# Kernel tuning notes

Hardware: AMD Instinct MI355X
Metric: run time of the kernel (lower is better)

## Reference

```python
import jax, jax.numpy as jnp
import numpy as np

EPS = 1e-5
K = 20
MAXV = 64


def knn_idx(x, k):
    # x: [B,N,D] -> idx: [B,N,k] (excluding self, matching torch topk of -dist)
    xx = jnp.sum(x * x, axis=-1, keepdims=True)                      # [B,N,1]
    dist = xx - 2.0 * jnp.einsum('bnd,bmd->bnm', x, x) + jnp.swapaxes(xx, 1, 2)
    _, idx = jax.lax.top_k(-dist, k + 1)
    return idx[:, :, 1:]


def edge_conv(x, W, gamma, beta, mean, var, k):
    # x: [B,N,C]; W: [O,2C]; BN in eval mode; max over k neighbors
    idx = knn_idx(x, k)                                              # [B,N,k]
    nbr = jax.vmap(lambda xi, ii: xi[ii])(x, idx)                    # [B,N,k,C]
    ctr = jnp.broadcast_to(x[:, :, None, :], nbr.shape)
    ef = jnp.concatenate([ctr, nbr - ctr], axis=-1)                  # [B,N,k,2C]
    y = jnp.einsum('bnkc,oc->bnko', ef, W)                           # 1x1 conv
    y = (y - mean) * (gamma * jax.lax.rsqrt(var + EPS)) + beta       # BN eval
    y = jnp.where(y >= 0, y, 0.2 * y)                                # LeakyReLU
    return jnp.max(y, axis=2)                                        # [B,N,O]


def setup_inputs() -> dict:
    key = jax.random.key(0)
    ks = jax.random.split(key, 32)
    f32 = jnp.float32
    def w(k_, o, i):
        return jax.random.normal(k_, (o, i), f32) / np.float32(np.sqrt(i))
    def vec(k_, c):
        return jax.random.normal(k_, (c,), f32) * 0.1
    d = {}
    d['x'] = jax.random.normal(ks[0], (4, 8192, 5), f32)
    # EdgeConv 1: 5 -> 32
    d['W1'] = w(ks[1], 32, 10)
    d['g1'] = jax.random.uniform(ks[2], (32,), f32, 0.5, 1.5)
    d['b1'] = vec(ks[3], 32); d['m1'] = vec(ks[4], 32)
    d['v1'] = jax.random.uniform(ks[5], (32,), f32, 0.5, 1.5)
    # EdgeConv 2: 32 -> 64
    d['W2'] = w(ks[6], 64, 64)
    d['g2'] = jax.random.uniform(ks[7], (64,), f32, 0.5, 1.5)
    d['b2'] = vec(ks[8], 64); d['m2'] = vec(ks[9], 64)
    d['v2'] = jax.random.uniform(ks[10], (64,), f32, 0.5, 1.5)
    # EdgeConv 3: 64 -> 128
    d['W3'] = w(ks[11], 128, 128)
    d['g3'] = jax.random.uniform(ks[12], (128,), f32, 0.5, 1.5)
    d['b3'] = vec(ks[13], 128); d['m3'] = vec(ks[14], 128)
    d['v3'] = jax.random.uniform(ks[15], (128,), f32, 0.5, 1.5)
    # conv_global: 224 -> 256
    d['Wg'] = w(ks[16], 256, 224)
    d['gg'] = jax.random.uniform(ks[17], (256,), f32, 0.5, 1.5)
    d['bg'] = vec(ks[18], 256); d['mg'] = vec(ks[19], 256)
    d['vg'] = jax.random.uniform(ks[20], (256,), f32, 0.5, 1.5)
    # vertex predictor heads
    d['Wv1'] = w(ks[21], 512, 256); d['bv1'] = vec(ks[22], 512)
    d['Wv2'] = w(ks[23], 192, 512); d['bv2'] = vec(ks[24], 192)
    d['Wq1'] = w(ks[25], 64, 256); d['bq1'] = vec(ks[26], 64)
    d['Wq2'] = w(ks[27], 1, 64); d['bq2'] = vec(ks[28], 1)
    return d


def reference(x, W1, g1, b1, m1, v1, W2, g2, b2, m2, v2, W3, g3, b3, m3, v3,
              Wg, gg, bg, mg, vg, Wv1, bv1, Wv2, bv2, Wq1, bq1, Wq2, bq2):
    B = x.shape[0]
    x1 = edge_conv(x, W1, g1, b1, m1, v1, K)      # [B,N,32]
    x2 = edge_conv(x1, W2, g2, b2, m2, v2, K)     # [B,N,64]
    x3 = edge_conv(x2, W3, g3, b3, m3, v3, K)     # [B,N,128]
    x_concat = jnp.concatenate([x1, x2, x3], axis=2)               # [B,N,224]
    xg = jnp.einsum('bnc,oc->bno', x_concat, Wg)                   # 1x1 conv1d
    xg = (xg - mg) * (gg * jax.lax.rsqrt(vg + EPS)) + bg
    xg = jnp.where(xg >= 0, xg, 0.2 * xg)
    gfeat = jnp.max(xg, axis=1)                                    # [B,256]
    h = jax.nn.relu(gfeat @ Wv1.T + bv1)                           # Dropout=eval id
    vertex_coords = (h @ Wv2.T + bv2).reshape(B, MAXV, 3)
    q = jax.nn.relu(gfeat @ Wq1.T + bq1)
    nvs = jax.nn.sigmoid(q @ Wq2.T + bq2)                          # [B,1]
    num_vertices = jnp.clip(jnp.round(nvs * MAXV), 1, MAXV).astype(jnp.int32)
    return (vertex_coords, num_vertices[:, 0], nvs[:, 0], gfeat, x_concat)
```

## Files before the change

### kernel.cpp

```cpp
#include <hip/hip_runtime.h>
#include <hip/hip_bf16.h>


#define NPTS 8192
#define BATCH 4
#define KNBR 20

template <int D, int RS, int S, int TJ, int B>
__global__ __launch_bounds__(128, 2) void knn_part(
    const float* feat, float* xcat) {
    constexpr bool PRE = (D % 4 == 0);
    __shared__ float xj[TJ * D];
    __shared__ float xxj[TJ];
    __shared__ float bufd[PRE ? 1 : B * 128];
    __shared__ unsigned short bufj[B * 128];
    const int JC = NPTS / S;

    int gi = blockIdx.x * 128 + threadIdx.x;
    int s  = blockIdx.y;
    int b  = gi >> 13;
    int ib = gi & (NPTS - 1);
    const float* fb = feat + (size_t)b * NPTS * RS;
    int tid = threadIdx.x;

    float xi[D];
    if (PRE) {
        #pragma unroll
        for (int c4 = 0; c4 < D / 4; ++c4) {
            float4 v = *(const float4*)(fb + (size_t)ib * RS + 4 * c4);
            xi[4 * c4] = v.x; xi[4 * c4 + 1] = v.y;
            xi[4 * c4 + 2] = v.z; xi[4 * c4 + 3] = v.w;
        }
    } else {
        #pragma unroll
        for (int c = 0; c < D; ++c) xi[c] = fb[(size_t)ib * RS + c];
    }
    float xxi = 0.f;
    #pragma unroll
    for (int c = 0; c < D; ++c) xxi = fmaf(xi[c], xi[c], xxi);

    float dl[21];
    int   il[21];
    #pragma unroll
    for (int t = 0; t < 21; ++t) { dl[t] = __builtin_inff(); il[t] = 0; }

    float thr = __builtin_inff();
    int   cnt = 0;
    int   j0  = 0;
    const float EPS = 1.52587890625e-05f;

    auto insP = [&](int u) {
        if (u < cnt) {
            int j  = (int)bufj[u * 128 + tid];
            int jl = j - j0;
            const float* row = xj + (size_t)jl * D;
            int fsw = jl & 7;
            float dot = 0.f;
            #pragma unroll
            for (int c4 = 0; c4 < D / 4; ++c4) {
                float4 v = *(const float4*)(row + ((c4 ^ fsw) * 4));
                dot = fmaf(xi[4 * c4 + 0], v.x, dot);
                dot = fmaf(xi[4 * c4 + 1], v.y, dot);
                dot = fmaf(xi[4 * c4 + 2], v.z, dot);
                dot = fmaf(xi[4 * c4 + 3], v.w, dot);
            }
            float dd = __builtin_fmaf(-2.f, dot, xxi + xxj[jl]);
            if (dd < dl[20]) {
                dl[20] = dd; il[20] = j;
                #pragma unroll
                for (int t = 20; t > 0; --t) {
                    if (dl[t] < dl[t - 1]) {
                        float td = dl[t]; dl[t] = dl[t - 1]; dl[t - 1] = td;
                        int   ti = il[t]; il[t] = il[t - 1]; il[t - 1] = ti;
                    }
                }
            }
        }
    };
    auto drainP = [&]() {
        #pragma unroll 1
        for (int u = 0; __any(u < cnt); u += 2) {
            insP(u);
            insP(u + 1);
        }
        cnt = 0;
        thr = dl[20];
    };
    auto drainR12 = [&]() {
        #pragma unroll 1
        for (int u = 0; __any(u < cnt); ++u) {
            if (u < cnt) {
                float dd  = bufd[u * 128 + tid];
                int   jj2 = (int)bufj[u * 128 + tid];
                if (dd < dl[20]) {
                    dl[20] = dd; il[20] = jj2;
                    #pragma unroll
                    for (int t = 20; t > 0; --t) {
                        if (dl[t] < dl[t - 1]) {
                            float td = dl[t]; dl[t] = dl[t - 1]; dl[t - 1] = td;
                            int   ti = il[t]; il[t] = il[t - 1]; il[t - 1] = ti;
                        }
                    }
                }
            }
        }
        cnt = 0;
        thr = dl[20];
    };

    #pragma unroll 1
    for (int t0 = s * JC; t0 < (s + 1) * JC; t0 += TJ) {
        j0 = t0;
        __syncthreads();
        if (PRE) {
            for (int e = tid; e < TJ * (D / 4); e += 128) {
                int r = e / (D / 4), c4 = e % (D / 4);
                float4 v = *(const float4*)(fb + (size_t)(t0 + r) * RS + 4 * c4);
                *(float4*)(xj + (size_t)r * D + (((c4 ^ (r & 7))) * 4)) = v;
            }
        } else {
            for (int e = tid; e < TJ * D; e += 128) {
                int r = e / D, c = e % D;
                xj[e] = fb[(size_t)(t0 + r) * RS + c];
            }
        }
        if (tid < TJ) {
            const float* row = fb + (size_t)(t0 + tid) * RS;
            float sm = 0.f;
            if (PRE) {
                #pragma unroll
                for (int c4 = 0; c4 < D / 4; ++c4) {
                    float4 v = *(const float4*)(row + 4 * c4);
                    sm = fmaf(v.x, v.x, sm); sm = fmaf(v.y, v.y, sm);
                    sm = fmaf(v.z, v.z, sm); sm = fmaf(v.w, v.w, sm);
                }
            } else {
                #pragma unroll
                for (int c = 0; c < D; ++c) sm = fmaf(row[c], row[c], sm);
            }
            xxj[tid] = sm;
        }
        __syncthreads();

        if (PRE) {
            #pragma unroll 1
            for (int jj = 0; jj < TJ; ++jj) {
                float sum = xxi + xxj[jj];
                const float* xr = xj + (size_t)jj * D;
                int fsw = jj & 7;
                float a0 = 0.f, a1 = 0.f, a2 = 0.f, a3 = 0.f;
                #pragma unroll
                for (int c4 = 0; c4 < D / 4; ++c4) {
                    float4 v = *(const float4*)(xr + ((c4 ^ fsw) * 4));
                    a0 = fmaf(xi[4 * c4 + 0], v.x, a0);
                    a1 = fmaf(xi[4 * c4 + 1], v.y, a1);
                    a2 = fmaf(xi[4 * c4 + 2], v.z, a2);
                    a3 = fmaf(xi[4 * c4 + 3], v.w, a3);
                }
                float dot4 = ((a0 + a1) + a2) + a3;
                float da = __builtin_fmaf(-2.f, dot4, sum);
                if (__any(cnt == B)) drainP();
                if (da < __builtin_fmaf(EPS, sum, thr)) {
                    bufj[cnt * 128 + tid] = (unsigned short)(t0 + jj);
                    ++cnt;
                }
            }
            drainP();
        } else {
            #pragma unroll 1
            for (int jj = 0; jj < TJ; ++jj) {
                float dot = 0.f;
                #pragma unroll
                for (int c = 0; c < D; ++c) dot = fmaf(xi[c], xj[jj * D + c], dot);
                float d = __builtin_fmaf(-2.f, dot, xxi + xxj[jj]);
                if (__any(cnt == B)) drainR12();
                if (d < thr) {
                    bufd[cnt * 128 + tid] = d;
                    bufj[cnt * 128 + tid] = (unsigned short)(t0 + jj);
                    ++cnt;
                }
            }
        }
    }
    if (!PRE) drainR12();

    unsigned short* cp =
        (unsigned short*)(xcat + (size_t)gi * 224 + 96) + s * 21;
    #pragma unroll
    for (int t = 0; t < 21; ++t) cp[t] = (unsigned short)il[t];
}

template <int D, int RS, int S>
__global__ __launch_bounds__(256) void knn_merge(
    const float* feat, const float* xcat, unsigned short* __restrict__ idxout) {
    int gi = blockIdx.x * 256 + threadIdx.x;
    int b  = gi >> 13;
    int ib = gi & (NPTS - 1);
    const float* fb = feat + (size_t)b * NPTS * RS;

    float xi[D];
    if (D % 4 == 0) {
        #pragma unroll
        for (int c4 = 0; c4 < D / 4; ++c4) {
            float4 v = *(const float4*)(fb + (size_t)ib * RS + 4 * c4);
            xi[4 * c4] = v.x; xi[4 * c4 + 1] = v.y;
            xi[4 * c4 + 2] = v.z; xi[4 * c4 + 3] = v.w;
        }
    } else {
        #pragma unroll
        for (int c = 0; c < D; ++c) xi[c] = fb[(size_t)ib * RS + c];
    }
    float xxi = 0.f;
    #pragma unroll
    for (int c = 0; c < D; ++c) xxi = fmaf(xi[c], xi[c], xxi);

    const unsigned short* cp =
        (const unsigned short*)(xcat + (size_t)gi * 224 + 96);

    float dl[21];
    int   il[21];
    #pragma unroll
    for (int t = 0; t < 21; ++t) { dl[t] = __builtin_inff(); il[t] = 0; }

    for (int t = 0; t < S * 21; ++t) {
        int j = ((int)cp[t]) & (NPTS - 1);
        const float* row = fb + (size_t)j * RS;
        float dot = 0.f, xx = 0.f;
        if (D % 4 == 0) {
            #pragma unroll
            for (int c4 = 0; c4 < D / 4; ++c4) {
                float4 v = *(const float4*)(row + 4 * c4);
                dot = fmaf(xi[4 * c4], v.x, dot);     xx = fmaf(v.x, v.x, xx);
                dot = fmaf(xi[4 * c4 + 1], v.y, dot); xx = fmaf(v.y, v.y, xx);
                dot = fmaf(xi[4 * c4 + 2], v.z, dot); xx = fmaf(v.z, v.z, xx);
                dot = fmaf(xi[4 * c4 + 3], v.w, dot); xx = fmaf(v.w, v.w, xx);
            }
        } else {
            #pragma unroll
            for (int c = 0; c < D; ++c) {
                float v = row[c];
                dot = fmaf(xi[c], v, dot);
                xx  = fmaf(v, v, xx);
            }
        }
        float d = __builtin_fmaf(-2.f, dot, xxi + xx);
        if (d < dl[20]) {
            dl[20] = d; il[20] = j;
            #pragma unroll
            for (int u = 20; u > 0; --u) {
                if (dl[u] < dl[u - 1]) {
                    float td = dl[u]; dl[u] = dl[u - 1]; dl[u - 1] = td;
                    int   ti = il[u]; il[u] = il[u - 1]; il[u - 1] = ti;
                }
            }
        }
    }
    unsigned short* op = idxout + (size_t)gi * KNBR;
    #pragma unroll
    for (int t = 1; t < 21; ++t) op[t - 1] = (unsigned short)il[t];
}

template <int CIN, int RS, int COUT, int OTILE, int P>
__global__ __launch_bounds__(256) void edgeconv_kernel(
    const float* feat, const unsigned short* __restrict__ knn,
    const float* __restrict__ W, const float* __restrict__ g,
    const float* __restrict__ beta, const float* __restrict__ mu,
    const float* __restrict__ var,
    float* outb, int concat_off) {
    __shared__ float diff[P][KNBR][CIN];
    __shared__ float xil[P][CIN];
    __shared__ unsigned short kidx[P * KNBR];
    __shared__ float sl[OTILE], bl[OTILE], ml[OTILE];

    int tid = threadIdx.x;
    int h   = blockIdx.y;
    int n0  = blockIdx.x * P;
    int b   = n0 >> 13;
    const float* fbase = feat + ((size_t)b << 13) * RS;

    for (int e = tid; e < P * CIN; e += 256)
        xil[e / CIN][e % CIN] = feat[(size_t)(n0 + e / CIN) * RS + e % CIN];
    for (int e = tid; e < P * KNBR; e += 256)
        kidx[e] = knn[(size_t)(n0 + e / KNBR) * KNBR + e % KNBR] & (NPTS - 1);
    for (int e = tid; e < OTILE; e += 256) {
        int o = h * OTILE + e;
        sl[e] = g[o] * rsqrtf(var[o] + 1e-5f);
        bl[e] = beta[o];
        ml[e] = mu[o];
    }
    __syncthreads();

    if (CIN % 4 == 0) {
        for (int e = tid; e < P * KNBR * (CIN / 4); e += 256) {
            int r = e / (CIN / 4), c4 = e % (CIN / 4);
            int p = r / KNBR, k = r % KNBR;
            int j = (int)kidx[r];
            float4 v = *(const float4*)(fbase + (size_t)j * RS + 4 * c4);
            diff[p][k][4 * c4 + 0] = v.x - xil[p][4 * c4 + 0];
            diff[p][k][4 * c4 + 1] = v.y - xil[p][4 * c4 + 1];
            diff[p][k][4 * c4 + 2] = v.z - xil[p][4 * c4 + 2];
            diff[p][k][4 * c4 + 3] = v.w - xil[p][4 * c4 + 3];
        }
    } else {
        for (int e = tid; e < P * KNBR * CIN; e += 256) {
            int r = e / CIN, c = e % CIN;
            int pp = r / KNBR, k = r % KNBR;
            int j = (int)kidx[r];
            diff[pp][k][c] = fbase[(size_t)j * RS + c] - xil[pp][c];
        }
    }
    __syncthreads();

    int ol = tid % OTILE, p = tid / OTILE;
    int o  = h * OTILE + ol;

    float wreg[CIN];
    #pragma unroll
    for (int c = 0; c < CIN; ++c) wreg[c] = W[(size_t)o * (2 * CIN) + c];
    float a = 0.f;
    #pragma unroll
    for (int c = 0; c < CIN; ++c) a = fmaf(wreg[c], xil[p][c], a);
    #pragma unroll
    for (int c = 0; c < CIN; ++c) wreg[c] = W[(size_t)o * (2 * CIN) + CIN + c];

    float s = sl[ol], mm = ml[ol], bb = bl[ol];
    float best = -__builtin_inff();
    for (int k = 0; k < KNBR; ++k) {
        float ac0 = a, ac1 = 0.f, ac2 = 0.f, ac3 = 0.f;
        #pragma unroll
        for (int c = 0; c < CIN; ++c) {
            float d = diff[p][k][c];
            if ((c & 3) == 0)      ac0 = fmaf(wreg[c], d, ac0);
            else if ((c & 3) == 1) ac1 = fmaf(wreg[c], d, ac1);
            else if ((c & 3) == 2) ac2 = fmaf(wreg[c], d, ac2);
            else                   ac3 = fmaf(wreg[c], d, ac3);
        }
        float acc = ((ac0 + ac1) + ac2) + ac3;
        float y = (acc - mm) * s + bb;
        y = (y >= 0.f) ? y : 0.2f * y;
        best = fmaxf(best, y);
    }
    outb[(size_t)(n0 + p) * 224 + concat_off + o] = best;
}

__global__ __launch_bounds__(256) void convglobal_kernel(
    const float* __restrict__ xcat,
    const float* __restrict__ Wg, const float* __restrict__ gg,
    const float* __restrict__ bg, const float* __restrict__ mg,
    const float* __restrict__ vg,
    float* __restrict__ partial) {
    const int KC = 56, PT = 64, OT = 64, ST = 68;
    __shared__ float flT[KC * ST];
    __shared__ float WlT[KC * ST];
    __shared__ float red[64 * 17];

    int tid = threadIdx.x;
    int oi  = tid & 15, pi = tid >> 4;
    int o0  = blockIdx.y * OT;
    int n0  = blockIdx.x * PT;
    int b   = n0 >> 13;
    int pchunk = blockIdx.x & 127;

    float acc[4][4];
    #pragma unroll
    for (int u = 0; u < 4; ++u)
        #pragma unroll
        for (int v = 0; v < 4; ++v) acc[u][v] = 0.f;

    for (int kc = 0; kc < 224; kc += KC) {
        __syncthreads();
        for (int e = tid; e < PT * (KC / 4); e += 256) {
            int p = e / (KC / 4), c4 = e % (KC / 4);
            float4 v = *(const float4*)(xcat + (size_t)(n0 + p) * 224 + kc + 4 * c4);
            flT[(4 * c4 + 0) * ST + p] = v.x;
            flT[(4 * c4 + 1) * ST + p] = v.y;
            flT[(4 * c4 + 2) * ST + p] = v.z;
            flT[(4 * c4 + 3) * ST + p] = v.w;
        }
        for (int e = tid; e < OT * (KC / 4); e += 256) {
            int o = e / (KC / 4), c4 = e % (KC / 4);
            float4 v = *(const float4*)(Wg + (size_t)(o0 + o) * 224 + kc + 4 * c4);
            WlT[(4 * c4 + 0) * ST + o] = v.x;
            WlT[(4 * c4 + 1) * ST + o] = v.y;
            WlT[(4 * c4 + 2) * ST + o] = v.z;
            WlT[(4 * c4 + 3) * ST + o] = v.w;
        }
        __syncthreads();
        #pragma unroll 8
        for (int c = 0; c < KC; ++c) {
            float4 w4 = *(const float4*)(WlT + c * ST + oi * 4);
            float4 f4 = *(const float4*)(flT + c * ST + pi * 4);
            acc[0][0] = fmaf(w4.x, f4.x, acc[0][0]);
            acc[0][1] = fmaf(w4.x, f4.y, acc[0][1]);
            acc[0][2] = fmaf(w4.x, f4.z, acc[0][2]);
            acc[0][3] = fmaf(w4.x, f4.w, acc[0][3]);
            acc[1][0] = fmaf(w4.y, f4.x, acc[1][0]);
            acc[1][1] = fmaf(w4.y, f4.y, acc[1][1]);
            acc[1][2] = fmaf(w4.y, f4.z, acc[1][2]);
            acc[1][3] = fmaf(w4.y, f4.w, acc[1][3]);
            acc[2][0] = fmaf(w4.z, f4.x, acc[2][0]);
            acc[2][1] = fmaf(w4.z, f4.y, acc[2][1]);
            acc[2][2] = fmaf(w4.z, f4.z, acc[2][2]);
            acc[2][3] = fmaf(w4.z, f4.w, acc[2][3]);
            acc[3][0] = fmaf(w4.w, f4.x, acc[3][0]);
            acc[3][1] = fmaf(w4.w, f4.y, acc[3][1]);
            acc[3][2] = fmaf(w4.w, f4.z, acc[3][2]);
            acc[3][3] = fmaf(w4.w, f4.w, acc[3][3]);
        }
    }
    #pragma unroll
    for (int u = 0; u < 4; ++u) {
        int oL = oi * 4 + u, o = o0 + oL;
        float s = gg[o] * rsqrtf(vg[o] + 1e-5f);
        float mm = mg[o], bb = bg[o];
        float best = -__builtin_inff();
        #pragma unroll
        for (int v = 0; v < 4; ++v) {
            float y = (acc[u][v] - mm) * s + bb;
            y = (y >= 0.f) ? y : 0.2f * y;
            best = fmaxf(best, y);
        }
        red[oL * 17 + pi] = best;
    }
    __syncthreads();
    if (tid < 64) {
        float best = -__builtin_inff();
        #pragma unroll
        for (int q = 0; q < 16; ++q) best = fmaxf(best, red[tid * 17 + q]);
        partial[((size_t)(b * 128 + pchunk)) * 256 + o0 + tid] = best;
    }
}

__global__ void reduce_gfeat_kernel(const float* __restrict__ partial,
                                    float* __restrict__ gfeat,
                                    float* __restrict__ outg) {
    int b = blockIdx.x, o = threadIdx.x;
    float best = -__builtin_inff();
    for (int ch = 0; ch < 128; ++ch)
        best = fmaxf(best, partial[((size_t)b * 128 + ch) * 256 + o]);
    gfeat[b * 256 + o] = best;
    outg[b * 256 + o]  = best;
}

__global__ __launch_bounds__(256) void heads_kernel(
    const float* __restrict__ gfeat,
    const float* __restrict__ Wv1, const float* __restrict__ bv1,
    const float* __restrict__ Wv2, const float* __restrict__ bv2,
    const float* __restrict__ Wq1, const float* __restrict__ bq1,
    const float* __restrict__ Wq2, const float* __restrict__ bq2,
    float* __restrict__ out) {
    int b = blockIdx.x, t = threadIdx.x;
    __shared__ float gf[256], h[512], q[64];
    gf[t] = gfeat[b * 256 + t];
    __syncthreads();
    for (int r = t; r < 512; r += 256) {
        float acc = bv1[r];
        for (int c = 0; c < 256; ++c) acc = fmaf(Wv1[r * 256 + c], gf[c], acc);
        h[r] = fmaxf(acc, 0.f);
    }
    __syncthreads();
    if (t < 192) {
        float acc = bv2[t];
        for (int c = 0; c < 512; ++c) acc = fmaf(Wv2[t * 512 + c], h[c], acc);
        out[b * 192 + t] = acc;
    } else {
        int r = t - 192;
        if (r < 64) {
            float acc = bq1[r];
            for (int c = 0; c < 256; ++c) acc = fmaf(Wq1[r * 256 + c], gf[c], acc);
            q[r] = fmaxf(acc, 0.f);
        }
    }
    __syncthreads();
    if (t == 0) {
        float acc = bq2[0];
        for (int c = 0; c < 64; ++c) acc = fmaf(Wq2[c], q[c], acc);
        float nv = 1.0f / (1.0f + expf(-acc));
        out[772 + b] = nv;
        float num = fminf(fmaxf(rintf(nv * 64.0f), 1.0f), 64.0f);
        out[768 + b] = num;
    }
}

extern "C" void kernel_launch(void* const* d_in, const int* in_sizes, int n_in,
                              void* d_out, int out_size, void* d_ws, size_t ws_size,
                              hipStream_t stream) {
    (void)in_sizes; (void)n_in; (void)out_size; (void)ws_size;
    const float* x   = (const float*)d_in[0];
    const float* W1  = (const float*)d_in[1];
    const float* g1  = (const float*)d_in[2];
    const float* b1  = (const float*)d_in[3];
    const float* m1  = (const float*)d_in[4];
    const float* v1  = (const float*)d_in[5];
    const float* W2  = (const float*)d_in[6];
    const float* g2  = (const float*)d_in[7];
    const float* b2  = (const float*)d_in[8];
    const float* m2  = (const float*)d_in[9];
    const float* v2  = (const float*)d_in[10];
    const float* W3  = (const float*)d_in[11];
    const float* g3  = (const float*)d_in[12];
    const float* b3  = (const float*)d_in[13];
    const float* m3  = (const float*)d_in[14];
    const float* v3  = (const float*)d_in[15];
    const float* Wg  = (const float*)d_in[16];
    const float* gg  = (const float*)d_in[17];
    const float* bg  = (const float*)d_in[18];
    const float* mg  = (const float*)d_in[19];
    const float* vg  = (const float*)d_in[20];
    const float* Wv1 = (const float*)d_in[21];
    const float* bv1 = (const float*)d_in[22];
    const float* Wv2 = (const float*)d_in[23];
    const float* bv2 = (const float*)d_in[24];
    const float* Wq1 = (const float*)d_in[25];
    const float* bq1 = (const float*)d_in[26];
    const float* Wq2 = (const float*)d_in[27];
    const float* bq2 = (const float*)d_in[28];

    float* out  = (float*)d_out;
    float* xcat = out + 1800;
    char* ws = (char*)d_ws;
    const int ROWS = BATCH * NPTS;

    unsigned short* idx  = (unsigned short*)(ws);
    float*          part = (float*)(ws);
    float*          gft  = (float*)(ws + 524288);

    knn_part<5, 5, 8, 128, 8><<<dim3(ROWS / 128, 8), 128, 0, stream>>>(x, xcat);
    knn_merge<5, 5, 8><<<ROWS / 256, 256, 0, stream>>>(x, xcat, idx);
    edgeconv_kernel<5, 5, 32, 32, 8>
        <<<dim3(ROWS / 8, 1), 256, 0, stream>>>(x, idx, W1, g1, b1, m1, v1, xcat, 0);

    knn_part<32, 224, 8, 128, 16><<<dim3(ROWS / 128, 8), 128, 0, stream>>>(xcat, xcat);
    knn_merge<32, 224, 8><<<ROWS / 256, 256, 0, stream>>>(xcat, xcat, idx);
    edgeconv_kernel<32, 224, 64, 64, 4>
        <<<dim3(ROWS / 4, 1), 256, 0, stream>>>(xcat, idx, W2, g2, b2, m2, v2, xcat, 32);

    knn_part<64, 224, 8, 64, 16><<<dim3(ROWS / 128, 8), 128, 0, stream>>>(xcat + 32, xcat);
    knn_merge<64, 224, 8><<<ROWS / 256, 256, 0, stream>>>(xcat + 32, xcat, idx);
    edgeconv_kernel<64, 224, 128, 64, 4>
        <<<dim3(ROWS / 4, 2), 256, 0, stream>>>(xcat + 32, idx, W3, g3, b3, m3, v3, xcat, 96);

    convglobal_kernel<<<dim3(ROWS / 64, 4), 256, 0, stream>>>(
        xcat, Wg, gg, bg, mg, vg, part);
    reduce_gfeat_kernel<<<BATCH, 256, 0, stream>>>(part, gft, out + 776);

    heads_kernel<<<BATCH, 256, 0, stream>>>(
        gft, Wv1, bv1, Wv2, bv2, Wq1, bq1, Wq2, bq2, out);
}
```

Baseline: 4.309 ms.

## Replace per-candidate top-k insertion with distance-only chain plus candidate ring buffer

For feature dims divisible by four, the partial kNN pass now keeps a sorted list of distances only (no indices) and pushes candidates within a precision margin of the current 20th distance into a per-thread shared-memory ring. The ring is compacted when nearly full. Surviving local indices, or an overflow marker, are written to scratch, and the merge kernel recomputes exact distances only for those candidates. It also processes two neighbours per iteration and shrinks merge blocks to 128 threads. The aim is to drop the index-swapping and recompute-on-drain work of the old buffered insertion, at the cost of more divergent ring bookkeeping and a full-chunk rescan whenever a thread overflows.

```diff
diff --git a/kernel.cpp b/kernel.cpp
--- a/kernel.cpp
+++ b/kernel.cpp
@@ -6,14 +6,18 @@
 #define BATCH 4
 #define KNBR 20
 
-template <int D, int RS, int S, int TJ, int B>
+template <int D, int RS, int S, int TJ, int M>
 __global__ __launch_bounds__(128, 2) void knn_part(
     const float* feat, float* xcat) {
     constexpr bool PRE = (D % 4 == 0);
+    constexpr int B5 = 8;
     __shared__ float xj[TJ * D];
     __shared__ float xxj[TJ];
-    __shared__ float bufd[PRE ? 1 : B * 128];
-    __shared__ unsigned short bufj[B * 128];
+    __shared__ float ringd[PRE ? M * 128 : 1];
+    __shared__ unsigned short ringj[PRE ? M * 128 : 1];
+    __shared__ float rmax[128];
+    __shared__ float bufd[PRE ? 1 : B5 * 128];
+    __shared__ unsigned short bufj[PRE ? 1 : B5 * 128];
     const int JC = NPTS / S;
 
     int gi = blockIdx.x * 128 + threadIdx.x;
@@ -22,6 +26,7 @@
     int ib = gi & (NPTS - 1);
     const float* fb = feat + (size_t)b * NPTS * RS;
     int tid = threadIdx.x;
+    const int sbase = s * JC;
 
     float xi[D];
     if (PRE) {
@@ -39,141 +44,192 @@
     #pragma unroll
     for (int c = 0; c < D; ++c) xxi = fmaf(xi[c], xi[c], xxi);
 
-    float dl[21];
-    int   il[21];
-    #pragma unroll
-    for (int t = 0; t < 21; ++t) { dl[t] = __builtin_inff(); il[t] = 0; }
-
-    float thr = __builtin_inff();
-    int   cnt = 0;
-    int   j0  = 0;
-    const float EPS = 1.52587890625e-05f;
-
-    auto insP = [&](int u) {
-        if (u < cnt) {
-            int j  = (int)bufj[u * 128 + tid];
-            int jl = j - j0;
-            const float* row = xj + (size_t)jl * D;
-            int fsw = jl & 7;
-            float dot = 0.f;
+    unsigned short* sc16 =
+        (unsigned short*)(xcat + (size_t)gi * 224 + 96) + s * 32;
+
+    if (PRE) {
+        float mx = 0.f;
+        for (int r = tid; r < JC; r += 128) {
+            const float* row = fb + (size_t)(sbase + r) * RS;
+            float sm = 0.f;
             #pragma unroll
             for (int c4 = 0; c4 < D / 4; ++c4) {
-                float4 v = *(const float4*)(row + ((c4 ^ fsw) * 4));
-                dot = fmaf(xi[4 * c4 + 0], v.x, dot);
-                dot = fmaf(xi[4 * c4 + 1], v.y, dot);
-                dot = fmaf(xi[4 * c4 + 2], v.z, dot);
-                dot = fmaf(xi[4 * c4 + 3], v.w, dot);
-            }
-            float dd = __builtin_fmaf(-2.f, dot, xxi + xxj[jl]);
-            if (dd < dl[20]) {
-                dl[20] = dd; il[20] = j;
+                float4 v = *(const float4*)(row + 4 * c4);
+                sm = fmaf(v.x, v.x, sm); sm = fmaf(v.y, v.y, sm);
+                sm = fmaf(v.z, v.z, sm); sm = fmaf(v.w, v.w, sm);
+            }
+            mx = fmaxf(mx, sm);
+        }
+        rmax[tid] = mx;
+        __syncthreads();
+        #pragma unroll
+        for (int off = 64; off >= 1; off >>= 1) {
+            if (tid < off) rmax[tid] = fmaxf(rmax[tid], rmax[tid + off]);
+            __syncthreads();
+        }
+        const float marg = 6.103515625e-05f * (xxi + rmax[0]);
+
+        float a[21];
+        #pragma unroll
+        for (int t = 0; t < 21; ++t) a[t] = __builtin_inff();
+        auto chain = [&](float v) {
+            if (v < a[20]) {
+                a[20] = v;
                 #pragma unroll
-                for (int t = 20; t > 0; --t) {
-                    if (dl[t] < dl[t - 1]) {
-                        float td = dl[t]; dl[t] = dl[t - 1]; dl[t - 1] = td;
-                        int   ti = il[t]; il[t] = il[t - 1]; il[t - 1] = ti;
+                for (int t = 20; t > 0; --t)
+                    if (a[t] < a[t - 1]) {
+                        float tv = a[t]; a[t] = a[t - 1]; a[t - 1] = tv;
                     }
-                }
-            }
-        }
-    };
-    auto drainP = [&]() {
+            }
+        };
+
+        int  cnt = 0;
+        bool ovf = false;
+        auto compactAll = [&]() {
+            float thr_c = a[20] + marg;
+            int nc = 0;
+            #pragma unroll 1
+            for (int u = 0; u < M; ++u) {
+                if (u < cnt) {
+                    float dv = ringd[u * 128 + tid];
+                    if (dv < thr_c) {
+                        if (nc != u) {
+                            ringd[nc * 128 + tid] = dv;
+                            ringj[nc * 128 + tid] = ringj[u * 128 + tid];
+                        }
+                        ++nc;
+                    }
+                }
+            }
+            cnt = nc;
+        };
+
         #pragma unroll 1
-        for (int u = 0; __any(u < cnt); u += 2) {
-            insP(u);
-            insP(u + 1);
-        }
-        cnt = 0;
-        thr = dl[20];
-    };
-    auto drainR12 = [&]() {
-        #pragma unroll 1
-        for (int u = 0; __any(u < cnt); ++u) {
-            if (u < cnt) {
-                float dd  = bufd[u * 128 + tid];
-                int   jj2 = (int)bufj[u * 128 + tid];
-                if (dd < dl[20]) {
-                    dl[20] = dd; il[20] = jj2;
-                    #pragma unroll
-                    for (int t = 20; t > 0; --t) {
-                        if (dl[t] < dl[t - 1]) {
-                            float td = dl[t]; dl[t] = dl[t - 1]; dl[t - 1] = td;
-                            int   ti = il[t]; il[t] = il[t - 1]; il[t - 1] = ti;
-                        }
-                    }
-                }
-            }
-        }
-        cnt = 0;
-        thr = dl[20];
-    };
-
-    #pragma unroll 1
-    for (int t0 = s * JC; t0 < (s + 1) * JC; t0 += TJ) {
-        j0 = t0;
-        __syncthreads();
-        if (PRE) {
+        for (int t0 = sbase; t0 < sbase + JC; t0 += TJ) {
+            __syncthreads();
             for (int e = tid; e < TJ * (D / 4); e += 128) {
                 int r = e / (D / 4), c4 = e % (D / 4);
                 float4 v = *(const float4*)(fb + (size_t)(t0 + r) * RS + 4 * c4);
                 *(float4*)(xj + (size_t)r * D + (((c4 ^ (r & 7))) * 4)) = v;
             }
-        } else {
-            for (int e = tid; e < TJ * D; e += 128) {
-                int r = e / D, c = e % D;
-                xj[e] = fb[(size_t)(t0 + r) * RS + c];
-            }
-        }
-        if (tid < TJ) {
-            const float* row = fb + (size_t)(t0 + tid) * RS;
-            float sm = 0.f;
-            if (PRE) {
+            if (tid < TJ) {
+                const float* row = fb + (size_t)(t0 + tid) * RS;
+                float sm = 0.f;
                 #pragma unroll
                 for (int c4 = 0; c4 < D / 4; ++c4) {
                     float4 v = *(const float4*)(row + 4 * c4);
                     sm = fmaf(v.x, v.x, sm); sm = fmaf(v.y, v.y, sm);
                     sm = fmaf(v.z, v.z, sm); sm = fmaf(v.w, v.w, sm);
                 }
-            } else {
-                #pragma unroll
-                for (int c = 0; c < D; ++c) sm = fmaf(row[c], row[c], sm);
-            }
-            xxj[tid] = sm;
-        }
-        __syncthreads();
-
-        if (PRE) {
+                xxj[tid] = sm;
+            }
+            __syncthreads();
+
+            int tl = t0 - sbase;
             #pragma unroll 1
-            for (int jj = 0; jj < TJ; ++jj) {
-                float sum = xxi + xxj[jj];
-                const float* xr = xj + (size_t)jj * D;
-                int fsw = jj & 7;
+            for (int jj = 0; jj < TJ; jj += 2) {
+                const float* xr0 = xj + (size_t)jj * D;
+                const float* xr1 = xr0 + D;
+                int f0 = jj & 7, f1 = (jj + 1) & 7;
                 float a0 = 0.f, a1 = 0.f, a2 = 0.f, a3 = 0.f;
+                float b0 = 0.f, b1 = 0.f, b2 = 0.f, b3 = 0.f;
                 #pragma unroll
                 for (int c4 = 0; c4 < D / 4; ++c4) {
-                    float4 v = *(const float4*)(xr + ((c4 ^ fsw) * 4));
+                    float4 v = *(const float4*)(xr0 + ((c4 ^ f0) * 4));
+                    float4 w = *(const float4*)(xr1 + ((c4 ^ f1) * 4));
                     a0 = fmaf(xi[4 * c4 + 0], v.x, a0);
                     a1 = fmaf(xi[4 * c4 + 1], v.y, a1);
                     a2 = fmaf(xi[4 * c4 + 2], v.z, a2);
                     a3 = fmaf(xi[4 * c4 + 3], v.w, a3);
-                }
-                float dot4 = ((a0 + a1) + a2) + a3;
-                float da = __builtin_fmaf(-2.f, dot4, sum);
-                if (__any(cnt == B)) drainP();
-                if (da < __builtin_fmaf(EPS, sum, thr)) {
-                    bufj[cnt * 128 + tid] = (unsigned short)(t0 + jj);
-                    ++cnt;
-                }
-            }
-            drainP();
+                    b0 = fmaf(xi[4 * c4 + 0], w.x, b0);
+                    b1 = fmaf(xi[4 * c4 + 1], w.y, b1);
+                    b2 = fmaf(xi[4 * c4 + 2], w.z, b2);
+                    b3 = fmaf(xi[4 * c4 + 3], w.w, b3);
+                }
+                float dot0 = ((a0 + a1) + a2) + a3;
+                float dot1 = ((b0 + b1) + b2) + b3;
+                float da0 = __builtin_fmaf(-2.f, dot0, xxi + xxj[jj]);
+                float da1 = __builtin_fmaf(-2.f, dot1, xxi + xxj[jj + 1]);
+                chain(da0);
+                chain(da1);
+                float thr_a = a[20] + marg;
+                bool w0 = da0 < thr_a, w1 = da1 < thr_a;
+                if (__any((w0 || w1) && cnt >= M - 2)) compactAll();
+                if (w0) {
+                    if (cnt < M) {
+                        ringd[cnt * 128 + tid] = da0;
+                        ringj[cnt * 128 + tid] = (unsigned short)(tl + jj);
+                        ++cnt;
+                    } else ovf = true;
+                }
+                if (w1) {
+                    if (cnt < M) {
+                        ringd[cnt * 128 + tid] = da1;
+                        ringj[cnt * 128 + tid] = (unsigned short)(tl + jj + 1);
+                        ++cnt;
+                    } else ovf = true;
+                }
+            }
+        }
+        compactAll();
+        if (ovf) {
+            sc16[0] = 0xFFFFu;
         } else {
+            sc16[0] = (unsigned short)cnt;
+            #pragma unroll 1
+            for (int k = 0; k < cnt; ++k) sc16[1 + k] = ringj[k * 128 + tid];
+        }
+    } else {
+        float dl[21];
+        int   il[21];
+        #pragma unroll
+        for (int t = 0; t < 21; ++t) { dl[t] = __builtin_inff(); il[t] = 0; }
+        float thr = __builtin_inff();
+        int   cnt = 0;
+        auto drainR12 = [&]() {
+            #pragma unroll 1
+            for (int u = 0; __any(u < cnt); ++u) {
+                if (u < cnt) {
+                    float dd  = bufd[u * 128 + tid];
+                    int   jj2 = (int)bufj[u * 128 + tid];
+                    if (dd < dl[20]) {
+                        dl[20] = dd; il[20] = jj2;
+                        #pragma unroll
+                        for (int t = 20; t > 0; --t) {
+                            if (dl[t] < dl[t - 1]) {
+                                float td = dl[t]; dl[t] = dl[t - 1]; dl[t - 1] = td;
+                                int   ti = il[t]; il[t] = il[t - 1]; il[t - 1] = ti;
+                            }
+                        }
+                    }
+                }
+            }
+            cnt = 0;
+            thr = dl[20];
+        };
+
+        #pragma unroll 1
+        for (int t0 = sbase; t0 < sbase + JC; t0 += TJ) {
+            __syncthreads();
+            for (int e = tid; e < TJ * D; e += 128) {
+                int r = e / D, c = e % D;
+                xj[e] = fb[(size_t)(t0 + r) * RS + c];
+            }
+            if (tid < TJ) {
+                const float* row = fb + (size_t)(t0 + tid) * RS;
+                float sm = 0.f;
+                #pragma unroll
+                for (int c = 0; c < D; ++c) sm = fmaf(row[c], row[c], sm);
+                xxj[tid] = sm;
+            }
+            __syncthreads();
             #pragma unroll 1
             for (int jj = 0; jj < TJ; ++jj) {
                 float dot = 0.f;
                 #pragma unroll
                 for (int c = 0; c < D; ++c) dot = fmaf(xi[c], xj[jj * D + c], dot);
                 float d = __builtin_fmaf(-2.f, dot, xxi + xxj[jj]);
-                if (__any(cnt == B)) drainR12();
+                if (__any(cnt == B5)) drainR12();
                 if (d < thr) {
                     bufd[cnt * 128 + tid] = d;
                     bufj[cnt * 128 + tid] = (unsigned short)(t0 + jj);
@@ -181,19 +237,19 @@
                 }
             }
         }
-    }
-    if (!PRE) drainR12();
-
-    unsigned short* cp =
-        (unsigned short*)(xcat + (size_t)gi * 224 + 96) + s * 21;
-    #pragma unroll
-    for (int t = 0; t < 21; ++t) cp[t] = (unsigned short)il[t];
+        drainR12();
+        sc16[0] = 21;
+        #pragma unroll
+        for (int t = 0; t < 21; ++t)
+            sc16[1 + t] = (unsigned short)(il[t] - sbase);
+    }
 }
 
 template <int D, int RS, int S>
-__global__ __launch_bounds__(256) void knn_merge(
+__global__ __launch_bounds__(128) void knn_merge(
     const float* feat, const float* xcat, unsigned short* __restrict__ idxout) {
-    int gi = blockIdx.x * 256 + threadIdx.x;
+    constexpr int JC = NPTS / S;
+    int gi = blockIdx.x * 128 + threadIdx.x;
     int b  = gi >> 13;
     int ib = gi & (NPTS - 1);
     const float* fb = feat + (size_t)b * NPTS * RS;
@@ -222,8 +278,7 @@
     #pragma unroll
     for (int t = 0; t < 21; ++t) { dl[t] = __builtin_inff(); il[t] = 0; }
 
-    for (int t = 0; t < S * 21; ++t) {
-        int j = ((int)cp[t]) & (NPTS - 1);
+    auto ins = [&](int j) {
         const float* row = fb + (size_t)j * RS;
         float dot = 0.f, xx = 0.f;
         if (D % 4 == 0) {
@@ -253,6 +308,19 @@
                     int   ti = il[u]; il[u] = il[u - 1]; il[u - 1] = ti;
                 }
             }
+        }
+    };
+
+    #pragma unroll 1
+    for (int s = 0; s < S; ++s) {
+        int cn = (int)cp[s * 32];
+        if (cn == 0xFFFF) {
+            #pragma unroll 1
+            for (int j = s * JC; j < (s + 1) * JC; ++j) ins(j);
+        } else {
+            #pragma unroll 1
+            for (int k = 0; k < cn; ++k)
+                ins(s * JC + ((int)cp[s * 32 + 1 + k] & (JC - 1)));
         }
     }
     unsigned short* op = idxout + (size_t)gi * KNBR;
@@ -525,18 +593,18 @@
     float*          part = (float*)(ws);
     float*          gft  = (float*)(ws + 524288);
 
-    knn_part<5, 5, 8, 128, 8><<<dim3(ROWS / 128, 8), 128, 0, stream>>>(x, xcat);
-    knn_merge<5, 5, 8><<<ROWS / 256, 256, 0, stream>>>(x, xcat, idx);
+    knn_part<5, 5, 8, 128, 28><<<dim3(ROWS / 128, 8), 128, 0, stream>>>(x, xcat);
+    knn_merge<5, 5, 8><<<ROWS / 128, 128, 0, stream>>>(x, xcat, idx);
     edgeconv_kernel<5, 5, 32, 32, 8>
         <<<dim3(ROWS / 8, 1), 256, 0, stream>>>(x, idx, W1, g1, b1, m1, v1, xcat, 0);
 
-    knn_part<32, 224, 8, 128, 16><<<dim3(ROWS / 128, 8), 128, 0, stream>>>(xcat, xcat);
-    knn_merge<32, 224, 8><<<ROWS / 256, 256, 0, stream>>>(xcat, xcat, idx);
+    knn_part<32, 224, 8, 128, 28><<<dim3(ROWS / 128, 8), 128, 0, stream>>>(xcat, xcat);
+    knn_merge<32, 224, 8><<<ROWS / 128, 128, 0, stream>>>(xcat, xcat, idx);
     edgeconv_kernel<32, 224, 64, 64, 4>
         <<<dim3(ROWS / 4, 1), 256, 0, stream>>>(xcat, idx, W2, g2, b2, m2, v2, xcat, 32);
 
-    knn_part<64, 224, 8, 64, 16><<<dim3(ROWS / 128, 8), 128, 0, stream>>>(xcat + 32, xcat);
-    knn_merge<64, 224, 8><<<ROWS / 256, 256, 0, stream>>>(xcat + 32, xcat, idx);
+    knn_part<64, 224, 8, 64, 28><<<dim3(ROWS / 128, 8), 128, 0, stream>>>(xcat + 32, xcat);
+    knn_merge<64, 224, 8><<<ROWS / 128, 128, 0, stream>>>(xcat + 32, xcat, idx);
     edgeconv_kernel<64, 224, 128, 64, 4>
         <<<dim3(ROWS / 4, 2), 256, 0, stream>>>(xcat + 32, idx, W3, g3, b3, m3, v3, xcat, 96);
 
```

Measured after the change: 5.726 ms. +32.9%, slower.
